# Kernel tuning notes

Measured on AMD Instinct MI355X. Metric: run time of the kernel, lower is better.

The kernel has to match this reference:

```python
import jax, jax.numpy as jnp
import numpy as np

D_MODEL = 768
D_STATE = 16
K_CONV = 4
BATCH = 2
SEQ = 2048


def setup_inputs() -> dict:
    key = jax.random.key(0)
    ks = jax.random.split(key, 16)
    dm, ds, K = D_MODEL, D_STATE, K_CONV
    s = 0.02
    inp = {
        "x": jax.random.normal(ks[0], (BATCH, SEQ, dm), dtype=jnp.float32),
        # linear weights stored (in, out); y = x @ W + b (equivalent to torch Linear)
        "Wi": jax.random.normal(ks[1], (dm, 2 * dm), dtype=jnp.float32) * s,
        "bi": jnp.zeros((2 * dm,), jnp.float32),
        "Wconv": jax.random.normal(ks[2], (dm, K), dtype=jnp.float32) * s,
        "bconv": jnp.zeros((dm,), jnp.float32),
        "Wdt": jax.random.normal(ks[3], (dm, dm), dtype=jnp.float32) * s,
        "bdt": jnp.zeros((dm,), jnp.float32),
        "WB": jax.random.normal(ks[4], (dm, dm * ds), dtype=jnp.float32) * s,
        "bB": jnp.zeros((dm * ds,), jnp.float32),
        "WC": jax.random.normal(ks[5], (dm, dm * ds), dtype=jnp.float32) * s,
        "bC": jnp.zeros((dm * ds,), jnp.float32),
        "A_log": jnp.zeros((dm, ds), jnp.float32),  # matches nn.Parameter(torch.zeros)
        "D": jnp.ones((dm,), jnp.float32),          # matches nn.Parameter(torch.ones)
        "Wo": jax.random.normal(ks[6], (dm, dm), dtype=jnp.float32) * s,
        "bo": jnp.zeros((dm,), jnp.float32),
    }
    return inp


def _forward(x, Wi, bi, Wconv, bconv, Wdt, bdt, WB, bB, WC, bC, A_log, D, Wo, bo):
    B, L, dm = x.shape
    ds = A_log.shape[1]
    K = Wconv.shape[1]

    uv = x @ Wi + bi                        # (B, L, 2*dm)
    u, v = uv[..., :dm], uv[..., dm:]

    # causal depthwise conv1d: torch pads K-1 both sides, keeps first L outputs
    u_pad = jnp.pad(u, ((0, 0), (K - 1, 0), (0, 0)))
    u_conv = bconv + sum(u_pad[:, k:k + L, :] * Wconv[:, k] for k in range(K))

    dt = jax.nn.softplus(u_conv @ Wdt + bdt)            # (B, L, dm)
    Bt = (u_conv @ WB + bB).reshape(B, L, dm, ds)       # (B, L, dm, ds)
    Ct = (u_conv @ WC + bC).reshape(B, L, dm, ds)
    A = -jnp.exp(A_log)                                  # (dm, ds)

    def step(s, inputs):
        dt_t, u_t, B_tt, C_tt = inputs                   # (B,dm), (B,dm), (B,dm,ds), (B,dm,ds)
        dt_e = dt_t[..., None]
        s = s * jnp.exp(dt_e * A) + dt_e * B_tt * u_t[..., None]
        y = jnp.sum(C_tt * s, axis=-1) + D * u_t         # (B, dm)
        return s, y

    s0 = jnp.zeros((B, dm, ds), x.dtype)
    xs = (dt.transpose(1, 0, 2), u_conv.transpose(1, 0, 2),
          Bt.transpose(1, 0, 2, 3), Ct.transpose(1, 0, 2, 3))
    _, ys = jax.lax.scan(step, s0, xs)                   # ys: (L, B, dm)
    y = ys.transpose(1, 0, 2)

    y = y * jax.nn.sigmoid(v)
    return y @ Wo + bo


def reference(x, Wi, bi, Wconv, bconv, Wdt, bdt, WB, bB, WC, bC, A_log, D, Wo, bo):
    return _forward(x, Wi, bi, Wconv, bconv, Wdt, bdt, WB, bB, WC, bC, A_log, D, Wo, bo)
```

## Files before the change

### kernel.cpp

```cpp
#include <hip/hip_runtime.h>

#define DM 768
#define DS 16
#define SEQ 2048
#define BATCH 2
#define MROWS (BATCH*SEQ)
#define N_UV (2*DM)
#define N_BC (DM*DS)
#define NGRP (BATCH*DM/4)
#define SUBMAX 64

typedef _Float16 half8 __attribute__((ext_vector_type(8)));
typedef float floatx4 __attribute__((ext_vector_type(4)));
typedef int i32x4 __attribute__((ext_vector_type(4)));
typedef unsigned short us8 __attribute__((ext_vector_type(8)));
typedef signed char c8 __attribute__((ext_vector_type(8)));

static __device__ __forceinline__ unsigned short f2h(float f) {
  _Float16 h = (_Float16)f;
  return __builtin_bit_cast(unsigned short, h);
}
static __device__ __forceinline__ float h2f(unsigned short u) {
  return (float)__builtin_bit_cast(_Float16, u);
}
static __device__ __forceinline__ float softplus_f(float x) {
  return (x > 20.f) ? x : log1pf(__expf(x));
}
static __device__ __forceinline__ void async_cp16(const void* g, void* l) {
  __builtin_amdgcn_global_load_lds(
      (const __attribute__((address_space(1))) void*)g,
      (__attribute__((address_space(3))) void*)l, 16, 0, 0);
}
static __device__ __forceinline__ float row_reduce16(float v) {
  int x;
  x = __builtin_amdgcn_update_dpp(0, __builtin_bit_cast(int, v), 0x128, 0xf, 0xf, true);
  v += __builtin_bit_cast(float, x);
  x = __builtin_amdgcn_update_dpp(0, __builtin_bit_cast(int, v), 0x124, 0xf, 0xf, true);
  v += __builtin_bit_cast(float, x);
  x = __builtin_amdgcn_update_dpp(0, __builtin_bit_cast(int, v), 0x122, 0xf, 0xf, true);
  v += __builtin_bit_cast(float, x);
  x = __builtin_amdgcn_update_dpp(0, __builtin_bit_cast(int, v), 0x121, 0xf, 0xf, true);
  v += __builtin_bit_cast(float, x);
  return v;
}

__global__ void convert_f2h(const float* __restrict__ in,
                            unsigned short* __restrict__ out, int n) {
  int i = (blockIdx.x * blockDim.x + threadIdx.x) * 4;
  if (i >= n) return;
  float4 f = *(const float4*)(in + i);
  ushort4 h;
  h.x = f2h(f.x); h.y = f2h(f.y); h.z = f2h(f.z); h.w = f2h(f.w);
  *(ushort4*)(out + i) = h;
}

__global__ void transpose_w5(const float* __restrict__ W0, const float* __restrict__ W1,
                             const float* __restrict__ W2, const float* __restrict__ W3,
                             const float* __restrict__ W4,
                             unsigned short* __restrict__ T0, unsigned short* __restrict__ T1,
                             unsigned short* __restrict__ T2, unsigned short* __restrict__ T3,
                             unsigned short* __restrict__ T4,
                             int N0, int N1, int N2, int N3, int N4) {
  const float* W; unsigned short* WT; int N;
  switch (blockIdx.z) {
    case 0: W = W0; WT = T0; N = N0; break;
    case 1: W = W1; WT = T1; N = N1; break;
    case 2: W = W2; WT = T2; N = N2; break;
    case 3: W = W3; WT = T3; N = N3; break;
    default: W = W4; WT = T4; N = N4; break;
  }
  int n0 = blockIdx.x * 32;
  if (n0 >= N) return;
  int k0 = blockIdx.y * 32;
  __shared__ float tile[32][33];
  int tx = threadIdx.x, ty = threadIdx.y;
#pragma unroll
  for (int i = 0; i < 32; i += 8)
    tile[ty + i][tx] = W[(size_t)(k0 + ty + i) * N + (n0 + tx)];
  __syncthreads();
  int kp = tx & 15, half = tx >> 4;
#pragma unroll
  for (int i = 0; i < 2; i++) {
    int nl = ty + half * 8 + i * 16;
    unsigned int pk = (unsigned int)f2h(tile[2 * kp][nl]) |
                      ((unsigned int)f2h(tile[2 * kp + 1][nl]) << 16);
    *(unsigned int*)&WT[(size_t)(n0 + nl) * DM + k0 + 2 * kp] = pk;
  }
}

__global__ __launch_bounds__(256)
void quant_rows(const unsigned short* __restrict__ in0,
                const unsigned short* __restrict__ in1,
                signed char* __restrict__ out0, signed char* __restrict__ out1,
                float* __restrict__ sc0, float* __restrict__ sc1, int R) {
  const unsigned short* in = blockIdx.y ? in1 : in0;
  signed char* out = blockIdx.y ? out1 : out0;
  float* scp = blockIdx.y ? sc1 : sc0;
  int row = blockIdx.x * 4 + (threadIdx.x >> 6);
  if (row >= R) return;
  int lane = threadIdx.x & 63;
  const us8* ch = (const us8*)(in + (size_t)row * DM);
  us8 a = ch[lane];
  us8 b = ch[64 + (lane & 31)];
  float fa[8], fb[8];
  float m = 0.f;
#pragma unroll
  for (int j = 0; j < 8; j++) { fa[j] = h2f(a[j]); m = fmaxf(m, fabsf(fa[j])); }
#pragma unroll
  for (int j = 0; j < 8; j++) fb[j] = h2f(b[j]);
  if (lane < 32) {
#pragma unroll
    for (int j = 0; j < 8; j++) m = fmaxf(m, fabsf(fb[j]));
  }
#pragma unroll
  for (int off = 32; off; off >>= 1) m = fmaxf(m, __shfl_xor(m, off));
  float inv = (m > 0.f) ? 127.f / m : 0.f;
  if (lane == 0) scp[row] = m * (1.f / 127.f);
  c8 qa, qb;
#pragma unroll
  for (int j = 0; j < 8; j++)
    qa[j] = (signed char)__float2int_rn(fminf(fmaxf(fa[j] * inv, -127.f), 127.f));
#pragma unroll
  for (int j = 0; j < 8; j++)
    qb[j] = (signed char)__float2int_rn(fminf(fmaxf(fb[j] * inv, -127.f), 127.f));
  c8* o = (c8*)(out + (size_t)row * DM);
  o[lane] = qa;
  if (lane < 32) o[64 + lane] = qb;
}

template<int ACT, int OUTH>
__global__ __launch_bounds__(256)
void gemm_f16(const unsigned short* __restrict__ A,
              const unsigned short* __restrict__ BT0,
              const unsigned short* __restrict__ BT1,
              const float* __restrict__ bias0,
              const float* __restrict__ bias1,
              void* __restrict__ Cout0,
              void* __restrict__ Cout1,
              int M, int N, int K, int TCa, int bstride, int row0) {
  const unsigned short* BT = blockIdx.z ? BT1 : BT0;
// ... 28 lines not shown
    async_cp16(Arow0 + k0, ldsA0);
    async_cp16(Arow1 + k0, ldsA1);
    async_cp16(Brow0 + k0, ldsB0);
    async_cp16(Brow1 + k0, ldsB1);
    __syncthreads();
    half8 af[4], bf[4];
#pragma unroll
    for (int i = 0; i < 4; i++) {
      af[i] = __builtin_bit_cast(half8, *(const uint4*)&As[(wm + i * 16 + l16) * 32 + pch]);
      bf[i] = __builtin_bit_cast(half8, *(const uint4*)&Bs[(wn + i * 16 + l16) * 32 + pch]);
    }
#pragma unroll
    for (int mi = 0; mi < 4; mi++)
#pragma unroll
      for (int ni = 0; ni < 4; ni++)
        acc[mi][ni] = __builtin_amdgcn_mfma_f32_16x16x32_f16(af[mi], bf[ni], acc[mi][ni], 0, 0, 0);
    __syncthreads();
  }

#pragma unroll
  for (int ni = 0; ni < 4; ni++) {
    int col = n0 + wn + ni * 16 + l16;
    float bv = bias[col];
#pragma unroll
    for (int mi = 0; mi < 4; mi++) {
#pragma unroll
      for (int r = 0; r < 4; r++) {
        int row = m0 + wm + mi * 16 + quad * 4 + r;
        float v = acc[mi][ni][r] + bv;
        if (ACT == 1) v = softplus_f(v);
        if (OUTH) ((unsigned short*)Cout)[(size_t)row * N + col] = f2h(v);
        else      ((float*)Cout)[(size_t)row * N + col] = v;
      }
    }
  }
}

__global__ __launch_bounds__(256)
void gemm_i8(const signed char* __restrict__ A,
             const signed char* __restrict__ BT0,
             const signed char* __restrict__ BT1,
             const float* __restrict__ bias0,
             const float* __restrict__ bias1,
             const float* __restrict__ sA,
             const float* __restrict__ sB0,
             const float* __restrict__ sB1,
             unsigned short* __restrict__ C0,
             unsigned short* __restrict__ C1,
             int M, int N, int K, int TCa, int bstride, int row0) {
  const signed char* BT = blockIdx.z ? BT1 : BT0;
  const float* bias = blockIdx.z ? bias1 : bias0;
  const float* sB = blockIdx.z ? sB1 : sB0;
  unsigned short* Cout = blockIdx.z ? C1 : C0;
  __shared__ __align__(16) signed char As[128 * 64];
  __shared__ __align__(16) signed char Bs[128 * 64];
  const int m0 = blockIdx.y * 128, n0 = blockIdx.x * 128;
  const int tid = threadIdx.x;
  const int lane = tid & 63, wave = tid >> 6;
  const int wm = (wave >> 1) * 64, wn = (wave & 1) * 64;
  const int l16 = lane & 15, quad = lane >> 4;
  const int sr = tid >> 2;
  const int sc = ((tid & 3) ^ ((tid >> 3) & 3)) * 16;
  const int pch = (quad ^ ((l16 >> 1) & 3)) * 16;

  i32x4 acc[4][4] = {};

  const int mA0 = m0 + sr, mA1 = m0 + sr + 64;
  const int gA0 = (mA0 / TCa) * bstride + row0 + (mA0 % TCa);
  const int gA1 = (mA1 / TCa) * bstride + row0 + (mA1 % TCa);
  const signed char* Arow0 = A + (size_t)gA0 * K + sc;
  const signed char* Arow1 = A + (size_t)gA1 * K + sc;
  const signed char* Brow0 = BT + (size_t)(n0 + sr) * K + sc;
  const signed char* Brow1 = BT + (size_t)(n0 + sr + 64) * K + sc;
  signed char* ldsA0 = As + (wave * 16) * 64;
  signed char* ldsA1 = As + (64 + wave * 16) * 64;
  signed char* ldsB0 = Bs + (wave * 16) * 64;
  signed char* ldsB1 = Bs + (64 + wave * 16) * 64;

  for (int k0 = 0; k0 < K; k0 += 64) {
    async_cp16(Arow0 + k0, ldsA0);
    async_cp16(Arow1 + k0, ldsA1);
    async_cp16(Brow0 + k0, ldsB0);
    async_cp16(Brow1 + k0, ldsB1);
    __syncthreads();
    i32x4 af[4], bf[4];
#pragma unroll
    for (int i = 0; i < 4; i++) {
      af[i] = *(const i32x4*)&As[(wm + i * 16 + l16) * 64 + pch];
      bf[i] = *(const i32x4*)&Bs[(wn + i * 16 + l16) * 64 + pch];
    }
#pragma unroll
    for (int mi = 0; mi < 4; mi++)
#pragma unroll
      for (int ni = 0; ni < 4; ni++)
        acc[mi][ni] = __builtin_amdgcn_mfma_i32_16x16x64_i8(af[mi], bf[ni], acc[mi][ni], 0, 0, 0);
    __syncthreads();
  }

  const int rowAbase = (m0 / TCa) * (bstride - TCa) + row0;
  float savs[4][4];
#pragma unroll
  for (int mi = 0; mi < 4; mi++)
#pragma unroll
    for (int r = 0; r < 4; r++)
      savs[mi][r] = sA[rowAbase + m0 + wm + mi * 16 + quad * 4 + r];

#pragma unroll
  for (int ni = 0; ni < 4; ni++) {
    int col = n0 + wn + ni * 16 + l16;
    float bv = bias[col];
    float sbv = sB[col];
#pragma unroll
    for (int mi = 0; mi < 4; mi++) {
#pragma unroll
      for (int r = 0; r < 4; r++) {
        int row = m0 + wm + mi * 16 + quad * 4 + r;
        float v = (float)acc[mi][ni][r] * (savs[mi][r] * sbv) + bv;
        Cout[(size_t)row * N + col] = f2h(v);
      }
    }
  }
}

__global__ void dwconv(const unsigned short* __restrict__ uv,
                       const float* __restrict__ Wconv,
                       const float* __restrict__ bconv,
                       unsigned short* __restrict__ uc) {
  int idx = blockIdx.x * 256 + threadIdx.x;
  int c = (idx % (DM / 2)) * 2;
  int row = idx / (DM / 2);
  int t = row & (SEQ - 1);
  float a0 = bconv[c], a1 = bconv[c + 1];
  const float* w0 = Wconv + c * 4;
  const float* w1 = Wconv + (c + 1) * 4;
#pragma unroll
  for (int k = 0; k < 4; k++) {
    int tt = t - 3 + k;
    if (tt >= 0) {
      ushort2 u2 = *(const ushort2*)&uv[(size_t)(row - 3 + k) * N_UV + c];
      a0 += h2f(u2.x) * w0[k];
      a1 += h2f(u2.y) * w1[k];
    }
  }
  ushort2 o; o.x = f2h(a0); o.y = f2h(a1);
  *(ushort2*)&uc[(size_t)row * DM + c] = o;
}

__global__ __launch_bounds__(64)
void scan_pass1(const unsigned short* __restrict__ dt,
                const unsigned short* __restrict__ uc,
                const unsigned short* __restrict__ Btc,
                const float* __restrict__ A_log,
                float* __restrict__ Ssub,
                float* __restrict__ Aexp,
                int ci, int TC, int SUBn) {
  const int TSUB = TC / SUBn;
  int wid = blockIdx.x, sub = blockIdx.y;
  int b = wid / (DM / 4);
  int c0 = (wid % (DM / 4)) * 4;
  int lane = threadIdx.x;
  int c = c0 + (lane >> 4);
  float Acj = -__expf(A_log[c0 * DS + lane]);
  int col = c0 * DS + lane;
  size_t gbase = (size_t)b * SEQ + (size_t)ci * TC + (size_t)sub * TSUB;
  size_t lbase = (size_t)b * TC + (size_t)sub * TSUB;

  float s = 0.f, dsum = 0.f;
  float n_dt[8], n_u[8], n_B[8];
#pragma unroll
  for (int i = 0; i < 8; i++) {
    n_dt[i] = h2f(dt[(gbase + i) * DM + c]);
    n_u[i]  = h2f(uc[(gbase + i) * DM + c]);
    n_B[i]  = h2f(Btc[(lbase + i) * N_BC + col]);
  }
  for (int t0 = 0; t0 < TSUB; t0 += 8) {
    float c_dt[8], c_u[8], c_B[8];
#pragma unroll
    for (int i = 0; i < 8; i++) { c_dt[i] = n_dt[i]; c_u[i] = n_u[i]; c_B[i] = n_B[i]; }
    if (t0 + 8 < TSUB) {
#pragma unroll
      for (int i = 0; i < 8; i++) {
        size_t gr = gbase + t0 + 8 + i, lr = lbase + t0 + 8 + i;
        n_dt[i] = h2f(dt[gr * DM + c]);
        n_u[i]  = h2f(uc[gr * DM + c]);
        n_B[i]  = h2f(Btc[lr * N_BC + col]);
      }
    }
#pragma unroll
    for (int i = 0; i < 8; i++) {
      float dtc = c_dt[i];
      dsum += dtc;
      float a = __expf(dtc * Acj);
      s = fmaf(s, a, dtc * c_B[i] * c_u[i]);
    }
  }
  int idx = (sub * BATCH + b) * N_BC + col;
  Ssub[idx] = s;
  Aexp[idx] = __expf(Acj * dsum);
}

template<int SUBN>
__global__ __launch_bounds__(64)
void scan_combine(const float* Ssub, const float* Aexp,
                  float* Sinit, float* s_state, int ci) {
  int wid = blockIdx.x;
  int b = wid / (DM / 4);
  int c0 = (wid % (DM / 4)) * 4;
  int col = c0 * DS + threadIdx.x;
  int sidx = b * N_BC + col;
  float sa[SUBN], ae[SUBN];
#pragma unroll
  for (int k = 0; k < SUBN; k++) {
    int idx = (k * BATCH + b) * N_BC + col;
    sa[k] = Ssub[idx];
    ae[k] = Aexp[idx];
  }
  float s = (ci == 0) ? 0.f : s_state[sidx];
#pragma unroll
  for (int k = 0; k < SUBN; k++) {
    int idx = (k * BATCH + b) * N_BC + col;
    Sinit[idx] = s;
    s = fmaf(s, ae[k], sa[k]);
  }
  s_state[sidx] = s;
}

__global__ __launch_bounds__(64)
void scan_pass2(const unsigned short* __restrict__ dt,
                const unsigned short* __restrict__ uc,
                const unsigned short* __restrict__ Btc,
                const unsigned short* __restrict__ Ctc,
                const unsigned short* __restrict__ uv,
                const float* __restrict__ A_log,
                const float* __restrict__ Dv,
                const float* __restrict__ Sinit,
                unsigned short* __restrict__ yg,
                int ci, int TC, int SUBn) {
  const int TSUB = TC / SUBn;
  int wid = blockIdx.x, sub = blockIdx.y;
  int b = wid / (DM / 4);
  int c0 = (wid % (DM / 4)) * 4;
  int lane = threadIdx.x;
  int j = lane & 15;
  int c = c0 + (lane >> 4);
  float Acj = -__expf(A_log[c0 * DS + lane]);
  float Dc = Dv[c];
  int col = c0 * DS + lane;
  float s = Sinit[(sub * BATCH + b) * N_BC + col];
  size_t gbase = (size_t)b * SEQ + (size_t)ci * TC + (size_t)sub * TSUB;
  size_t lbase = (size_t)b * TC + (size_t)sub * TSUB;

  float n_dt[8], n_u[8], n_B[8], n_C[8], n_v[8];
#pragma unroll
  for (int i = 0; i < 8; i++) {
    size_t gr = gbase + i, lr = lbase + i;
    n_dt[i] = h2f(dt[gr * DM + c]);
    n_u[i]  = h2f(uc[gr * DM + c]);
    n_B[i]  = h2f(Btc[lr * N_BC + col]);
    n_C[i]  = h2f(Ctc[lr * N_BC + col]);
    n_v[i]  = h2f(uv[gr * N_UV + DM + c]);
  }
  for (int t0 = 0; t0 < TSUB; t0 += 8) {
    float c_dt[8], c_u[8], c_B[8], c_C[8], c_v[8];
#pragma unroll
    for (int i = 0; i < 8; i++) {
      c_dt[i] = n_dt[i]; c_u[i] = n_u[i]; c_B[i] = n_B[i];
      c_C[i] = n_C[i]; c_v[i] = n_v[i];
    }
    if (t0 + 8 < TSUB) {
#pragma unroll
      for (int i = 0; i < 8; i++) {
        size_t gr = gbase + t0 + 8 + i, lr = lbase + t0 + 8 + i;
        n_dt[i] = h2f(dt[gr * DM + c]);
        n_u[i]  = h2f(uc[gr * DM + c]);
        n_B[i]  = h2f(Btc[lr * N_BC + col]);
        n_C[i]  = h2f(Ctc[lr * N_BC + col]);
        n_v[i]  = h2f(uv[gr * N_UV + DM + c]);
      }
    }
#pragma unroll
    for (int i = 0; i < 8; i++) {
      float dtc = c_dt[i];
      float a = __expf(dtc * Acj);
      s = fmaf(s, a, dtc * c_B[i] * c_u[i]);
      float yt = row_reduce16(c_C[i] * s);
      if (j == 0) {
        float y = yt + Dc * c_u[i];
        float g = 1.f / (1.f + __expf(-c_v[i]));
        yg[(gbase + t0 + i) * DM + c] = f2h(y * g);
      }
    }
  }
}

extern "C" void kernel_launch(void* const* d_in, const int* in_sizes, int n_in,
                              void* d_out, int out_size, void* d_ws, size_t ws_size,
                              hipStream_t stream) {
  const float* x     = (const float*)d_in[0];
  const float* Wi    = (const float*)d_in[1];
  const float* bi    = (const float*)d_in[2];
  const float* Wconv = (const float*)d_in[3];
  const float* bconv = (const float*)d_in[4];
  const float* Wdt   = (const float*)d_in[5];
  const float* bdt   = (const float*)d_in[6];
  const float* WB    = (const float*)d_in[7];
  const float* bB    = (const float*)d_in[8];
  const float* WC    = (const float*)d_in[9];
  const float* bC    = (const float*)d_in[10];
  const float* A_log = (const float*)d_in[11];
  const float* Dv    = (const float*)d_in[12];
  const float* Wo    = (const float*)d_in[13];
  const float* bo    = (const float*)d_in[14];
  float* out = (float*)d_out;
  (void)in_sizes; (void)n_in; (void)out_size;

  auto pad = [](size_t b) { return (b + 255) & ~(size_t)255; };

  const size_t sz_xb   = pad((size_t)MROWS * DM * 2);
  const size_t sz_WiT  = pad((size_t)N_UV * DM * 2);
  const size_t sz_WdtT = pad((size_t)DM * DM * 2);
  const size_t sz_WBT  = pad((size_t)N_BC * DM * 2);
  const size_t sz_WCT  = pad((size_t)N_BC * DM * 2);
  const size_t sz_WoT  = pad((size_t)DM * DM * 2);
  const size_t sz_uvb  = pad((size_t)MROWS * N_UV * 2);
  const size_t sz_ucb  = pad((size_t)MROWS * DM * 2);
  const size_t sz_dtb  = pad((size_t)MROWS * DM * 2);
  const size_t sz_st   = pad((size_t)BATCH * N_BC * 4);
  const size_t sz_sub  = pad((size_t)SUBMAX * BATCH * N_BC * 4);
  const size_t sz_uc8  = pad((size_t)MROWS * DM);
  const size_t sz_w8   = pad((size_t)N_BC * DM);
  const size_t sz_sA   = pad((size_t)MROWS * 4);
  const size_t sz_sB   = pad((size_t)N_BC * 4);
  const size_t fixed = sz_xb + sz_WiT + sz_WdtT + sz_WBT + sz_WCT + sz_WoT +
                       sz_uvb + sz_ucb + sz_dtb + sz_st + 2 * sz_sub +
                       sz_uc8 + 2 * sz_w8 + sz_sA + 2 * sz_sB;

  int NC = 16;
  for (int nc : {1, 2, 4, 8, 16}) {
    size_t need = fixed + 2 * pad((size_t)BATCH * (SEQ / nc) * N_BC * 2);
    if (need <= ws_size) { NC = nc; break; }
  }
  const int TC = SEQ / NC;
  const int MC = BATCH * TC;
  const int SUBn = (TC / 8 < SUBMAX) ? (TC / 8) : SUBMAX;

  char* ws = (char*)d_ws;
  size_t off = 0;
  auto alloc = [&](size_t bytes) { char* p = ws + off; off += bytes; return p; };
  unsigned short* xb   = (unsigned short*)alloc(sz_xb);
  unsigned short* WiT  = (unsigned short*)alloc(sz_WiT);
  unsigned short* WdtT = (unsigned short*)alloc(sz_WdtT);
  unsigned short* WBT  = (unsigned short*)alloc(sz_WBT);
  unsigned short* WCT  = (unsigned short*)alloc(sz_WCT);
  unsigned short* WoT  = (unsigned short*)alloc(sz_WoT);
  unsigned short* uvb  = (unsigned short*)alloc(sz_uvb);
  unsigned short* ucb  = (unsigned short*)alloc(sz_ucb);
  unsigned short* dtb  = (unsigned short*)alloc(sz_dtb);
  float*          sst  = (float*)alloc(sz_st);
  float*          Ssub = (float*)alloc(sz_sub);
  float*          Aexp = (float*)alloc(sz_sub);
  signed char*    uc8  = (signed char*)alloc(sz_uc8);
  signed char*    WBT8 = (signed char*)alloc(sz_w8);
  signed char*    WCT8 = (signed char*)alloc(sz_w8);
  float*          sAu  = (float*)alloc(sz_sA);
  float*          sB0  = (float*)alloc(sz_sB);
  float*          sB1  = (float*)alloc(sz_sB);
  unsigned short* Btc  = (unsigned short*)alloc(pad((size_t)MC * N_BC * 2));
  unsigned short* Ctc  = (unsigned short*)alloc(pad((size_t)MC * N_BC * 2));
  unsigned short* ygb  = xb;
  float*          Sini = Ssub;

  convert_f2h<<<dim3(MROWS * DM / 1024), dim3(256), 0, stream>>>(x, xb, MROWS * DM);
  transpose_w5<<<dim3(N_BC / 32, DM / 32, 5), dim3(32, 8), 0, stream>>>(
      Wi, Wdt, WB, WC, Wo, WiT, WdtT, WBT, WCT, WoT, N_UV, DM, N_BC, N_BC, DM);
  quant_rows<<<dim3(N_BC / 4, 2), 256, 0, stream>>>(WBT, WCT, WBT8, WCT8,
                                                    sB0, sB1, N_BC);

  gemm_f16<0, 1><<<dim3(N_UV / 128, MROWS / 128, 1), 256, 0, stream>>>(
      xb, WiT, WiT, bi, bi, uvb, uvb, MROWS, N_UV, DM, MROWS, 0, 0);
  dwconv<<<dim3(MROWS * DM / 512), 256, 0, stream>>>(uvb, Wconv, bconv, ucb);
  quant_rows<<<dim3(MROWS / 4, 1), 256, 0, stream>>>(ucb, ucb, uc8, uc8,
                                                     sAu, sAu, MROWS);
  gemm_f16<1, 1><<<dim3(DM / 128, MROWS / 128, 1), 256, 0, stream>>>(
      ucb, WdtT, WdtT, bdt, bdt, dtb, dtb, MROWS, DM, DM, MROWS, 0, 0);

  for (int ci = 0; ci < NC; ci++) {
    gemm_i8<<<dim3(N_BC / 128, MC / 128, 2), 256, 0, stream>>>(
        uc8, WBT8, WCT8, bB, bC, sAu, sB0, sB1, Btc, Ctc,
        MC, N_BC, DM, TC, SEQ, ci * TC);
    scan_pass1<<<dim3(NGRP, SUBn), 64, 0, stream>>>(dtb, ucb, Btc, A_log,
                                                    Ssub, Aexp, ci, TC, SUBn);
    switch (SUBn) {
      case 64: scan_combine<64><<<dim3(NGRP), 64, 0, stream>>>(Ssub, Aexp, Sini, sst, ci); break;
      case 32: scan_combine<32><<<dim3(NGRP), 64, 0, stream>>>(Ssub, Aexp, Sini, sst, ci); break;
      default: scan_combine<16><<<dim3(NGRP), 64, 0, stream>>>(Ssub, Aexp, Sini, sst, ci); break;
    }
    scan_pass2<<<dim3(NGRP, SUBn), 64, 0, stream>>>(dtb, ucb, Btc, Ctc, uvb,
                                                    A_log, Dv, Sini, ygb, ci, TC, SUBn);
  }

  gemm_f16<0, 0><<<dim3(DM / 128, MROWS / 128, 1), 256, 0, stream>>>(
      ygb, WoT, WoT, bo, bo, out, out, MROWS, DM, DM, MROWS, 0, 0);
}
```

Before: 553.6 us.

## Triple-buffer int8 GEMM LDS loads and vectorize transposed epilogue stores

```diff
diff --git a/kernel.cpp b/kernel.cpp
--- a/kernel.cpp
+++ b/kernel.cpp
@@ -15,6 +15,7 @@
 typedef int i32x4 __attribute__((ext_vector_type(4)));
 typedef unsigned short us8 __attribute__((ext_vector_type(8)));
 typedef signed char c8 __attribute__((ext_vector_type(8)));
+typedef __fp16 fp16x2 __attribute__((ext_vector_type(2)));
 
 static __device__ __forceinline__ unsigned short f2h(float f) {
   _Float16 h = (_Float16)f;
@@ -22,6 +23,10 @@
 }
 static __device__ __forceinline__ float h2f(unsigned short u) {
   return (float)__builtin_bit_cast(_Float16, u);
+}
+static __device__ __forceinline__ unsigned int pk2h(float a, float b) {
+  fp16x2 r = __builtin_amdgcn_cvt_pkrtz(a, b);
+  return __builtin_bit_cast(unsigned int, r);
 }
 static __device__ __forceinline__ float softplus_f(float x) {
   return (x > 20.f) ? x : log1pf(__expf(x));
@@ -220,8 +225,8 @@
   const float* bias = blockIdx.z ? bias1 : bias0;
   const float* sB = blockIdx.z ? sB1 : sB0;
   unsigned short* Cout = blockIdx.z ? C1 : C0;
-  __shared__ __align__(16) signed char As[128 * 64];
-  __shared__ __align__(16) signed char Bs[128 * 64];
+  __shared__ __align__(16) signed char As[3][128 * 64];
+  __shared__ __align__(16) signed char Bs[3][128 * 64];
   const int m0 = blockIdx.y * 128, n0 = blockIdx.x * 128;
   const int tid = threadIdx.x;
   const int lane = tid & 63, wave = tid >> 6;
@@ -240,52 +245,68 @@
   const signed char* Arow1 = A + (size_t)gA1 * K + sc;
   const signed char* Brow0 = BT + (size_t)(n0 + sr) * K + sc;
   const signed char* Brow1 = BT + (size_t)(n0 + sr + 64) * K + sc;
-  signed char* ldsA0 = As + (wave * 16) * 64;
-  signed char* ldsA1 = As + (64 + wave * 16) * 64;
-  signed char* ldsB0 = Bs + (wave * 16) * 64;
-  signed char* ldsB1 = Bs + (64 + wave * 16) * 64;
-
-  for (int k0 = 0; k0 < K; k0 += 64) {
-    async_cp16(Arow0 + k0, ldsA0);
-    async_cp16(Arow1 + k0, ldsA1);
-    async_cp16(Brow0 + k0, ldsB0);
-    async_cp16(Brow1 + k0, ldsB1);
-    __syncthreads();
+  const int woff = (wave * 16) * 64;
+
+  const int nt = K >> 6;
+  auto stage = [&](int t, int b) {
+    int k0 = t << 6;
+    async_cp16(Arow0 + k0, &As[b][woff]);
+    async_cp16(Arow1 + k0, &As[b][64 * 64 + woff]);
+    async_cp16(Brow0 + k0, &Bs[b][woff]);
+    async_cp16(Brow1 + k0, &Bs[b][64 * 64 + woff]);
+  };
+  stage(0, 0);
+  if (nt > 1) stage(1, 1);
+  int cur = 0;
+  for (int t = 0; t < nt; ++t) {
+    if (t + 2 < nt) {
+      int b2 = cur + 2; if (b2 >= 3) b2 -= 3;
+      stage(t + 2, b2);
+      asm volatile("s_waitcnt vmcnt(8)" ::: "memory");
+    } else if (t + 1 < nt) {
+      asm volatile("s_waitcnt vmcnt(4)" ::: "memory");
+    } else {
+      asm volatile("s_waitcnt vmcnt(0)" ::: "memory");
+    }
+    __builtin_amdgcn_s_barrier();
     i32x4 af[4], bf[4];
 #pragma unroll
     for (int i = 0; i < 4; i++) {
-      af[i] = *(const i32x4*)&As[(wm + i * 16 + l16) * 64 + pch];
-      bf[i] = *(const i32x4*)&Bs[(wn + i * 16 + l16) * 64 + pch];
-    }
+      af[i] = *(const i32x4*)&As[cur][(wm + i * 16 + l16) * 64 + pch];
+      bf[i] = *(const i32x4*)&Bs[cur][(wn + i * 16 + l16) * 64 + pch];
+    }
+    asm volatile("s_waitcnt lgkmcnt(0)" ::: "memory");
+    __builtin_amdgcn_s_barrier();
+    __builtin_amdgcn_s_setprio(1);
 #pragma unroll
     for (int mi = 0; mi < 4; mi++)
 #pragma unroll
       for (int ni = 0; ni < 4; ni++)
-        acc[mi][ni] = __builtin_amdgcn_mfma_i32_16x16x64_i8(af[mi], bf[ni], acc[mi][ni], 0, 0, 0);
-    __syncthreads();
+        acc[mi][ni] = __builtin_amdgcn_mfma_i32_16x16x64_i8(bf[ni], af[mi], acc[mi][ni], 0, 0, 0);
+    __builtin_amdgcn_s_setprio(0);
+    cur = (cur == 2) ? 0 : cur + 1;
   }
 
   const int rowAbase = (m0 / TCa) * (bstride - TCa) + row0;
-  float savs[4][4];
-#pragma unroll
-  for (int mi = 0; mi < 4; mi++)
-#pragma unroll
-    for (int r = 0; r < 4; r++)
-      savs[mi][r] = sA[rowAbase + m0 + wm + mi * 16 + quad * 4 + r];
-
-#pragma unroll
-  for (int ni = 0; ni < 4; ni++) {
-    int col = n0 + wn + ni * 16 + l16;
-    float bv = bias[col];
-    float sbv = sB[col];
-#pragma unroll
-    for (int mi = 0; mi < 4; mi++) {
-#pragma unroll
-      for (int r = 0; r < 4; r++) {
-        int row = m0 + wm + mi * 16 + quad * 4 + r;
-        float v = (float)acc[mi][ni][r] * (savs[mi][r] * sbv) + bv;
-        Cout[(size_t)row * N + col] = f2h(v);
-      }
+
+#pragma unroll
+  for (int mi = 0; mi < 4; mi++) {
+    int row = m0 + wm + mi * 16 + l16;
+    float sa = sA[rowAbase + row];
+    size_t outb = (size_t)row * N;
+#pragma unroll
+    for (int ni = 0; ni < 4; ni++) {
+      int nb = n0 + wn + ni * 16 + quad * 4;
+      float4 sb4 = *(const float4*)&sB[nb];
+      float4 bv4 = *(const float4*)&bias[nb];
+      float v0 = (float)acc[mi][ni][0] * (sa * sb4.x) + bv4.x;
+      float v1 = (float)acc[mi][ni][1] * (sa * sb4.y) + bv4.y;
+      float v2 = (float)acc[mi][ni][2] * (sa * sb4.z) + bv4.z;
+      float v3 = (float)acc[mi][ni][3] * (sa * sb4.w) + bv4.w;
+      uint2 pk;
+      pk.x = pk2h(v0, v1);
+      pk.y = pk2h(v2, v3);
+      *(uint2*)&Cout[outb + nb] = pk;
     }
   }
 }
```

After: 584.9 us. +5.7%, slower.

## Transpose scan activations to channel-major and vectorize int8 GEMM epilogue stores

Applied to the files above, without the earlier changes.

```diff
diff --git a/kernel.cpp b/kernel.cpp
--- a/kernel.cpp
+++ b/kernel.cpp
@@ -15,6 +15,7 @@
 typedef int i32x4 __attribute__((ext_vector_type(4)));
 typedef unsigned short us8 __attribute__((ext_vector_type(8)));
 typedef signed char c8 __attribute__((ext_vector_type(8)));
+typedef __fp16 fp16x2 __attribute__((ext_vector_type(2)));
 
 static __device__ __forceinline__ unsigned short f2h(float f) {
   _Float16 h = (_Float16)f;
@@ -22,6 +23,10 @@
 }
 static __device__ __forceinline__ float h2f(unsigned short u) {
   return (float)__builtin_bit_cast(_Float16, u);
+}
+static __device__ __forceinline__ unsigned int pk2h(float a, float b) {
+  fp16x2 r = __builtin_amdgcn_cvt_pkrtz(a, b);
+  return __builtin_bit_cast(unsigned int, r);
 }
 static __device__ __forceinline__ float softplus_f(float x) {
   return (x > 20.f) ? x : log1pf(__expf(x));
@@ -86,6 +91,30 @@
                       ((unsigned int)f2h(tile[2 * kp + 1][nl]) << 16);
     *(unsigned int*)&WT[(size_t)(n0 + nl) * DM + k0 + 2 * kp] = pk;
   }
+}
+
+__global__ void transpose_act3(const unsigned short* __restrict__ dt,
+                               const unsigned short* __restrict__ uc,
+                               const unsigned short* __restrict__ uv,
+                               unsigned short* __restrict__ dtT,
+                               unsigned short* __restrict__ ucT,
+                               unsigned short* __restrict__ vT) {
+  const unsigned short* src; unsigned short* dst; int ld, coff;
+  switch (blockIdx.z) {
+    case 0:  src = dt; dst = dtT; ld = DM;   coff = 0;  break;
+    case 1:  src = uc; dst = ucT; ld = DM;   coff = 0;  break;
+    default: src = uv; dst = vT;  ld = N_UV; coff = DM; break;
+  }
+  __shared__ unsigned short tile[32][33];
+  int r0 = blockIdx.x * 32, c0 = blockIdx.y * 32;
+  int tx = threadIdx.x, ty = threadIdx.y;
+#pragma unroll
+  for (int i = 0; i < 32; i += 8)
+    tile[ty + i][tx] = src[(size_t)(r0 + ty + i) * ld + coff + c0 + tx];
+  __syncthreads();
+#pragma unroll
+  for (int i = 0; i < 32; i += 8)
+    dst[(size_t)(c0 + ty + i) * MROWS + r0 + tx] = tile[tx][ty + i];
 }
 
 __global__ __launch_bounds__(256)
@@ -261,31 +290,30 @@
     for (int mi = 0; mi < 4; mi++)
 #pragma unroll
       for (int ni = 0; ni < 4; ni++)
-        acc[mi][ni] = __builtin_amdgcn_mfma_i32_16x16x64_i8(af[mi], bf[ni], acc[mi][ni], 0, 0, 0);
+        acc[mi][ni] = __builtin_amdgcn_mfma_i32_16x16x64_i8(bf[ni], af[mi], acc[mi][ni], 0, 0, 0);
     __syncthreads();
   }
 
   const int rowAbase = (m0 / TCa) * (bstride - TCa) + row0;
-  float savs[4][4];
-#pragma unroll
-  for (int mi = 0; mi < 4; mi++)
-#pragma unroll
-    for (int r = 0; r < 4; r++)
-      savs[mi][r] = sA[rowAbase + m0 + wm + mi * 16 + quad * 4 + r];
-
-#pragma unroll
-  for (int ni = 0; ni < 4; ni++) {
-    int col = n0 + wn + ni * 16 + l16;
-    float bv = bias[col];
-    float sbv = sB[col];
-#pragma unroll
-    for (int mi = 0; mi < 4; mi++) {
-#pragma unroll
-      for (int r = 0; r < 4; r++) {
-        int row = m0 + wm + mi * 16 + quad * 4 + r;
-        float v = (float)acc[mi][ni][r] * (savs[mi][r] * sbv) + bv;
-        Cout[(size_t)row * N + col] = f2h(v);
-      }
+
+#pragma unroll
+  for (int mi = 0; mi < 4; mi++) {
+    int row = m0 + wm + mi * 16 + l16;
+    float sa = sA[rowAbase + row];
+    size_t outb = (size_t)row * N;
+#pragma unroll
+    for (int ni = 0; ni < 4; ni++) {
+      int nb = n0 + wn + ni * 16 + quad * 4;
+      float4 sb4 = *(const float4*)&sB[nb];
+      float4 bv4 = *(const float4*)&bias[nb];
+      float v0 = (float)acc[mi][ni][0] * (sa * sb4.x) + bv4.x;
+      float v1 = (float)acc[mi][ni][1] * (sa * sb4.y) + bv4.y;
+      float v2 = (float)acc[mi][ni][2] * (sa * sb4.z) + bv4.z;
+      float v3 = (float)acc[mi][ni][3] * (sa * sb4.w) + bv4.w;
+      uint2 pk;
+      pk.x = pk2h(v0, v1);
+      pk.y = pk2h(v2, v3);
+      *(uint2*)&Cout[outb + nb] = pk;
     }
   }
 }
@@ -314,52 +342,53 @@
   *(ushort2*)&uc[(size_t)row * DM + c] = o;
 }
 
-__global__ __launch_bounds__(64)
-void scan_pass1(const unsigned short* __restrict__ dt,
-                const unsigned short* __restrict__ uc,
+__global__ __launch_bounds__(256)
+void scan_pass1(const unsigned short* __restrict__ dtT,
+                const unsigned short* __restrict__ ucT,
                 const unsigned short* __restrict__ Btc,
                 const float* __restrict__ A_log,
                 float* __restrict__ Ssub,
                 float* __restrict__ Aexp,
                 int ci, int TC, int SUBn) {
   const int TSUB = TC / SUBn;
-  int wid = blockIdx.x, sub = blockIdx.y;
+  int wid = blockIdx.x * 4 + (threadIdx.x >> 6);
+  int sub = blockIdx.y;
   int b = wid / (DM / 4);
   int c0 = (wid % (DM / 4)) * 4;
-  int lane = threadIdx.x;
+  int lane = threadIdx.x & 63;
   int c = c0 + (lane >> 4);
   float Acj = -__expf(A_log[c0 * DS + lane]);
   int col = c0 * DS + lane;
-  size_t gbase = (size_t)b * SEQ + (size_t)ci * TC + (size_t)sub * TSUB;
+  size_t tbase = (size_t)b * SEQ + (size_t)ci * TC + (size_t)sub * TSUB;
   size_t lbase = (size_t)b * TC + (size_t)sub * TSUB;
+  const unsigned short* dtp = dtT + (size_t)c * MROWS + tbase;
+  const unsigned short* ucp = ucT + (size_t)c * MROWS + tbase;
 
   float s = 0.f, dsum = 0.f;
-  float n_dt[8], n_u[8], n_B[8];
-#pragma unroll
-  for (int i = 0; i < 8; i++) {
-    n_dt[i] = h2f(dt[(gbase + i) * DM + c]);
-    n_u[i]  = h2f(uc[(gbase + i) * DM + c]);
-    n_B[i]  = h2f(Btc[(lbase + i) * N_BC + col]);
-  }
+  us8 ndt = *(const us8*)dtp;
+  us8 nuc = *(const us8*)ucp;
+  float n_B[8];
+#pragma unroll
+  for (int i = 0; i < 8; i++)
+    n_B[i] = h2f(Btc[(lbase + i) * N_BC + col]);
   for (int t0 = 0; t0 < TSUB; t0 += 8) {
-    float c_dt[8], c_u[8], c_B[8];
-#pragma unroll
-    for (int i = 0; i < 8; i++) { c_dt[i] = n_dt[i]; c_u[i] = n_u[i]; c_B[i] = n_B[i]; }
+    us8 cdt = ndt, cuc = nuc;
+    float c_B[8];
+#pragma unroll
+    for (int i = 0; i < 8; i++) c_B[i] = n_B[i];
     if (t0 + 8 < TSUB) {
-#pragma unroll
-      for (int i = 0; i < 8; i++) {
-        size_t gr = gbase + t0 + 8 + i, lr = lbase + t0 + 8 + i;
-        n_dt[i] = h2f(dt[gr * DM + c]);
-        n_u[i]  = h2f(uc[gr * DM + c]);
-        n_B[i]  = h2f(Btc[lr * N_BC + col]);
-      }
+      ndt = *(const us8*)&dtp[t0 + 8];
+      nuc = *(const us8*)&ucp[t0 + 8];
+#pragma unroll
+      for (int i = 0; i < 8; i++)
+        n_B[i] = h2f(Btc[(lbase + t0 + 8 + i) * N_BC + col]);
     }
 #pragma unroll
     for (int i = 0; i < 8; i++) {
-      float dtc = c_dt[i];
+      float dtc = h2f(cdt[i]);
       dsum += dtc;
       float a = __expf(dtc * Acj);
-      s = fmaf(s, a, dtc * c_B[i] * c_u[i]);
+      s = fmaf(s, a, dtc * c_B[i] * h2f(cuc[i]));
     }
   }
   int idx = (sub * BATCH + b) * N_BC + col;
@@ -368,13 +397,14 @@
 }
 
 template<int SUBN>
-__global__ __launch_bounds__(64)
+__global__ __launch_bounds__(256)
 void scan_combine(const float* Ssub, const float* Aexp,
                   float* Sinit, float* s_state, int ci) {
-  int wid = blockIdx.x;
+  int wid = blockIdx.x * 4 + (threadIdx.x >> 6);
+  int lane = threadIdx.x & 63;
   int b = wid / (DM / 4);
   int c0 = (wid % (DM / 4)) * 4;
-  int col = c0 * DS + threadIdx.x;
+  int col = c0 * DS + lane;
   int sidx = b * N_BC + col;
   float sa[SUBN], ae[SUBN];
 #pragma unroll
@@ -393,69 +423,72 @@
   s_state[sidx] = s;
 }
 
-__global__ __launch_bounds__(64)
-void scan_pass2(const unsigned short* __restrict__ dt,
-                const unsigned short* __restrict__ uc,
+__global__ __launch_bounds__(256)
+void scan_pass2(const unsigned short* __restrict__ dtT,
+                const unsigned short* __restrict__ ucT,
                 const unsigned short* __restrict__ Btc,
                 const unsigned short* __restrict__ Ctc,
-                const unsigned short* __restrict__ uv,
+                const unsigned short* __restrict__ vT,
                 const float* __restrict__ A_log,
                 const float* __restrict__ Dv,
                 const float* __restrict__ Sinit,
                 unsigned short* __restrict__ yg,
                 int ci, int TC, int SUBn) {
   const int TSUB = TC / SUBn;
-  int wid = blockIdx.x, sub = blockIdx.y;
+  int wid = blockIdx.x * 4 + (threadIdx.x >> 6);
+  int sub = blockIdx.y;
   int b = wid / (DM / 4);
   int c0 = (wid % (DM / 4)) * 4;
-  int lane = threadIdx.x;
+  int lane = threadIdx.x & 63;
   int j = lane & 15;
   int c = c0 + (lane >> 4);
   float Acj = -__expf(A_log[c0 * DS + lane]);
   float Dc = Dv[c];
   int col = c0 * DS + lane;
   float s = Sinit[(sub * BATCH + b) * N_BC + col];
-  size_t gbase = (size_t)b * SEQ + (size_t)ci * TC + (size_t)sub * TSUB;
+  size_t tbase = (size_t)b * SEQ + (size_t)ci * TC + (size_t)sub * TSUB;
   size_t lbase = (size_t)b * TC + (size_t)sub * TSUB;
-
-  float n_dt[8], n_u[8], n_B[8], n_C[8], n_v[8];
+  const unsigned short* dtp = dtT + (size_t)c * MROWS + tbase;
+  const unsigned short* ucp = ucT + (size_t)c * MROWS + tbase;
+  const unsigned short* vp  = vT  + (size_t)c * MROWS + tbase;
+
+  us8 ndt = *(const us8*)dtp;
+  us8 nuc = *(const us8*)ucp;
+  us8 nv  = *(const us8*)vp;
+  float n_B[8], n_C[8];
 #pragma unroll
   for (int i = 0; i < 8; i++) {
-    size_t gr = gbase + i, lr = lbase + i;
-    n_dt[i] = h2f(dt[gr * DM + c]);
-    n_u[i]  = h2f(uc[gr * DM + c]);
-    n_B[i]  = h2f(Btc[lr * N_BC + col]);
-    n_C[i]  = h2f(Ctc[lr * N_BC + col]);
-    n_v[i]  = h2f(uv[gr * N_UV + DM + c]);
+    size_t lr = lbase + i;
+    n_B[i] = h2f(Btc[lr * N_BC + col]);
+    n_C[i] = h2f(Ctc[lr * N_BC + col]);
   }
   for (int t0 = 0; t0 < TSUB; t0 += 8) {
-    float c_dt[8], c_u[8], c_B[8], c_C[8], c_v[8];
+    us8 cdt = ndt, cuc = nuc, cv = nv;
+    float c_B[8], c_C[8];
+#pragma unroll
+    for (int i = 0; i < 8; i++) { c_B[i] = n_B[i]; c_C[i] = n_C[i]; }
+    if (t0 + 8 < TSUB) {
+      ndt = *(const us8*)&dtp[t0 + 8];
+      nuc = *(const us8*)&ucp[t0 + 8];
+      nv  = *(const us8*)&vp[t0 + 8];
+#pragma unroll
+      for (int i = 0; i < 8; i++) {
+        size_t lr = lbase + t0 + 8 + i;
+        n_B[i] = h2f(Btc[lr * N_BC + col]);
+        n_C[i] = h2f(Ctc[lr * N_BC + col]);
+      }
+    }
 #pragma unroll
     for (int i = 0; i < 8; i++) {
-      c_dt[i] = n_dt[i]; c_u[i] = n_u[i]; c_B[i] = n_B[i];
-      c_C[i] = n_C[i]; c_v[i] = n_v[i];
-    }
-    if (t0 + 8 < TSUB) {
-#pragma unroll
-      for (int i = 0; i < 8; i++) {
-        size_t gr = gbase + t0 + 8 + i, lr = lbase + t0 + 8 + i;
-        n_dt[i] = h2f(dt[gr * DM + c]);
-        n_u[i]  = h2f(uc[gr * DM + c]);
-        n_B[i]  = h2f(Btc[lr * N_BC + col]);
-        n_C[i]  = h2f(Ctc[lr * N_BC + col]);
-        n_v[i]  = h2f(uv[gr * N_UV + DM + c]);
-      }
-    }
-#pragma unroll
-    for (int i = 0; i < 8; i++) {
-      float dtc = c_dt[i];
+      float dtc = h2f(cdt[i]);
+      float uci = h2f(cuc[i]);
       float a = __expf(dtc * Acj);
-      s = fmaf(s, a, dtc * c_B[i] * c_u[i]);
+      s = fmaf(s, a, dtc * c_B[i] * uci);
       float yt = row_reduce16(c_C[i] * s);
       if (j == 0) {
-        float y = yt + Dc * c_u[i];
-        float g = 1.f / (1.f + __expf(-c_v[i]));
-        yg[(gbase + t0 + i) * DM + c] = f2h(y * g);
+        float y = yt + Dc * uci;
+        float g = 1.f / (1.f + __expf(-h2f(cv[i])));
+        yg[(tbase + t0 + i) * DM + c] = f2h(y * g);
       }
     }
   }
@@ -493,6 +526,7 @@
   const size_t sz_uvb  = pad((size_t)MROWS * N_UV * 2);
   const size_t sz_ucb  = pad((size_t)MROWS * DM * 2);
   const size_t sz_dtb  = pad((size_t)MROWS * DM * 2);
+  const size_t sz_actT = pad((size_t)DM * MROWS * 2);
   const size_t sz_st   = pad((size_t)BATCH * N_BC * 4);
   const size_t sz_sub  = pad((size_t)SUBMAX * BATCH * N_BC * 4);
   const size_t sz_uc8  = pad((size_t)MROWS * DM);
@@ -500,8 +534,8 @@
   const size_t sz_sA   = pad((size_t)MROWS * 4);
   const size_t sz_sB   = pad((size_t)N_BC * 4);
   const size_t fixed = sz_xb + sz_WiT + sz_WdtT + sz_WBT + sz_WCT + sz_WoT +
-                       sz_uvb + sz_ucb + sz_dtb + sz_st + 2 * sz_sub +
-                       sz_uc8 + 2 * sz_w8 + sz_sA + 2 * sz_sB;
+                       sz_uvb + sz_ucb + sz_dtb + 3 * sz_actT + sz_st +
+                       2 * sz_sub + sz_uc8 + 2 * sz_w8 + sz_sA + 2 * sz_sB;
 
   int NC = 16;
   for (int nc : {1, 2, 4, 8, 16}) {
@@ -524,6 +558,9 @@
   unsigned short* uvb  = (unsigned short*)alloc(sz_uvb);
   unsigned short* ucb  = (unsigned short*)alloc(sz_ucb);
   unsigned short* dtb  = (unsigned short*)alloc(sz_dtb);
+  unsigned short* dtT  = (unsigned short*)alloc(sz_actT);
+  unsigned short* ucT  = (unsigned short*)alloc(sz_actT);
+  unsigned short* vT   = (unsigned short*)alloc(sz_actT);
   float*          sst  = (float*)alloc(sz_st);
   float*          Ssub = (float*)alloc(sz_sub);
   float*          Aexp = (float*)alloc(sz_sub);
@@ -551,20 +588,22 @@
                                                      sAu, sAu, MROWS);
   gemm_f16<1, 1><<<dim3(DM / 128, MROWS / 128, 1), 256, 0, stream>>>(
       ucb, WdtT, WdtT, bdt, bdt, dtb, dtb, MROWS, DM, DM, MROWS, 0, 0);
+  transpose_act3<<<dim3(MROWS / 32, DM / 32, 3), dim3(32, 8), 0, stream>>>(
+      dtb, ucb, uvb, dtT, ucT, vT);
 
   for (int ci = 0; ci < NC; ci++) {
     gemm_i8<<<dim3(N_BC / 128, MC / 128, 2), 256, 0, stream>>>(
         uc8, WBT8, WCT8, bB, bC, sAu, sB0, sB1, Btc, Ctc,
         MC, N_BC, DM, TC, SEQ, ci * TC);
-    scan_pass1<<<dim3(NGRP, SUBn), 64, 0, stream>>>(dtb, ucb, Btc, A_log,
-                                                    Ssub, Aexp, ci, TC, SUBn);
+    scan_pass1<<<dim3(NGRP / 4, SUBn), 256, 0, stream>>>(dtT, ucT, Btc, A_log,
+                                                         Ssub, Aexp, ci, TC, SUBn);
     switch (SUBn) {
-      case 64: scan_combine<64><<<dim3(NGRP), 64, 0, stream>>>(Ssub, Aexp, Sini, sst, ci); break;
-      case 32: scan_combine<32><<<dim3(NGRP), 64, 0, stream>>>(Ssub, Aexp, Sini, sst, ci); break;
-      default: scan_combine<16><<<dim3(NGRP), 64, 0, stream>>>(Ssub, Aexp, Sini, sst, ci); break;
-    }
-    scan_pass2<<<dim3(NGRP, SUBn), 64, 0, stream>>>(dtb, ucb, Btc, Ctc, uvb,
-                                                    A_log, Dv, Sini, ygb, ci, TC, SUBn);
+      case 64: scan_combine<64><<<dim3(NGRP / 4), 256, 0, stream>>>(Ssub, Aexp, Sini, sst, ci); break;
+      case 32: scan_combine<32><<<dim3(NGRP / 4), 256, 0, stream>>>(Ssub, Aexp, Sini, sst, ci); break;
+      default: scan_combine<16><<<dim3(NGRP / 4), 256, 0, stream>>>(Ssub, Aexp, Sini, sst, ci); break;
+    }
+    scan_pass2<<<dim3(NGRP / 4, SUBn), 256, 0, stream>>>(dtT, ucT, Btc, Ctc, vT,
+                                                         A_log, Dv, Sini, ygb, ci, TC, SUBn);
   }
 
   gemm_f16<0, 0><<<dim3(DM / 128, MROWS / 128, 1), 256, 0, stream>>>(
```

After: 590.5 us. +6.7%, slower.

## Replace chunked three-pass scan with single sequential scan over transposed activations

Applied to the files above, without the earlier changes.

```diff
diff --git a/kernel.cpp b/kernel.cpp
--- a/kernel.cpp
+++ b/kernel.cpp
@@ -8,7 +8,6 @@
 #define N_UV (2*DM)
 #define N_BC (DM*DS)
 #define NGRP (BATCH*DM/4)
-#define SUBMAX 64
 
 typedef _Float16 half8 __attribute__((ext_vector_type(8)));
 typedef float floatx4 __attribute__((ext_vector_type(4)));
@@ -86,6 +85,30 @@
                       ((unsigned int)f2h(tile[2 * kp + 1][nl]) << 16);
     *(unsigned int*)&WT[(size_t)(n0 + nl) * DM + k0 + 2 * kp] = pk;
   }
+}
+
+__global__ void transpose_act3(const unsigned short* __restrict__ dt,
+                               const unsigned short* __restrict__ uc,
+                               const unsigned short* __restrict__ uv,
+                               unsigned short* __restrict__ dtT,
+                               unsigned short* __restrict__ ucT,
+                               unsigned short* __restrict__ vT) {
+  const unsigned short* src; unsigned short* dst; int ld, coff;
+  switch (blockIdx.z) {
+    case 0:  src = dt; dst = dtT; ld = DM;   coff = 0;  break;
+    case 1:  src = uc; dst = ucT; ld = DM;   coff = 0;  break;
+    default: src = uv; dst = vT;  ld = N_UV; coff = DM; break;
+  }
+  __shared__ unsigned short tile[32][33];
+  int r0 = blockIdx.x * 32, c0 = blockIdx.y * 32;
+  int tx = threadIdx.x, ty = threadIdx.y;
+#pragma unroll
+  for (int i = 0; i < 32; i += 8)
+    tile[ty + i][tx] = src[(size_t)(r0 + ty + i) * ld + coff + c0 + tx];
+  __syncthreads();
+#pragma unroll
+  for (int i = 0; i < 32; i += 8)
+    dst[(size_t)(c0 + ty + i) * MROWS + r0 + tx] = tile[tx][ty + i];
 }
 
 __global__ __launch_bounds__(256)
@@ -315,97 +338,17 @@
 }
 
 __global__ __launch_bounds__(64)
-void scan_pass1(const unsigned short* __restrict__ dt,
-                const unsigned short* __restrict__ uc,
-                const unsigned short* __restrict__ Btc,
-                const float* __restrict__ A_log,
-                float* __restrict__ Ssub,
-                float* __restrict__ Aexp,
-                int ci, int TC, int SUBn) {
-  const int TSUB = TC / SUBn;
-  int wid = blockIdx.x, sub = blockIdx.y;
-  int b = wid / (DM / 4);
-  int c0 = (wid % (DM / 4)) * 4;
-  int lane = threadIdx.x;
-  int c = c0 + (lane >> 4);
-  float Acj = -__expf(A_log[c0 * DS + lane]);
-  int col = c0 * DS + lane;
-  size_t gbase = (size_t)b * SEQ + (size_t)ci * TC + (size_t)sub * TSUB;
-  size_t lbase = (size_t)b * TC + (size_t)sub * TSUB;
-
-  float s = 0.f, dsum = 0.f;
-  float n_dt[8], n_u[8], n_B[8];
-#pragma unroll
-  for (int i = 0; i < 8; i++) {
-    n_dt[i] = h2f(dt[(gbase + i) * DM + c]);
-    n_u[i]  = h2f(uc[(gbase + i) * DM + c]);
-    n_B[i]  = h2f(Btc[(lbase + i) * N_BC + col]);
-  }
-  for (int t0 = 0; t0 < TSUB; t0 += 8) {
-    float c_dt[8], c_u[8], c_B[8];
-#pragma unroll
-    for (int i = 0; i < 8; i++) { c_dt[i] = n_dt[i]; c_u[i] = n_u[i]; c_B[i] = n_B[i]; }
-    if (t0 + 8 < TSUB) {
-#pragma unroll
-      for (int i = 0; i < 8; i++) {
-        size_t gr = gbase + t0 + 8 + i, lr = lbase + t0 + 8 + i;
-        n_dt[i] = h2f(dt[gr * DM + c]);
-        n_u[i]  = h2f(uc[gr * DM + c]);
-        n_B[i]  = h2f(Btc[lr * N_BC + col]);
-      }
-    }
-#pragma unroll
-    for (int i = 0; i < 8; i++) {
-      float dtc = c_dt[i];
-      dsum += dtc;
-      float a = __expf(dtc * Acj);
-      s = fmaf(s, a, dtc * c_B[i] * c_u[i]);
-    }
-  }
-  int idx = (sub * BATCH + b) * N_BC + col;
-  Ssub[idx] = s;
-  Aexp[idx] = __expf(Acj * dsum);
-}
-
-template<int SUBN>
-__global__ __launch_bounds__(64)
-void scan_combine(const float* Ssub, const float* Aexp,
-                  float* Sinit, float* s_state, int ci) {
+void scan_full(const unsigned short* __restrict__ dtT,
+               const unsigned short* __restrict__ ucT,
+               const unsigned short* __restrict__ vT,
+               const unsigned short* __restrict__ Btc,
+               const unsigned short* __restrict__ Ctc,
+               const float* __restrict__ A_log,
+               const float* __restrict__ Dv,
+               float* __restrict__ s_state,
+               unsigned short* __restrict__ yg,
+               int ci, int TC) {
   int wid = blockIdx.x;
-  int b = wid / (DM / 4);
-  int c0 = (wid % (DM / 4)) * 4;
-  int col = c0 * DS + threadIdx.x;
-  int sidx = b * N_BC + col;
-  float sa[SUBN], ae[SUBN];
-#pragma unroll
-  for (int k = 0; k < SUBN; k++) {
-    int idx = (k * BATCH + b) * N_BC + col;
-    sa[k] = Ssub[idx];
-    ae[k] = Aexp[idx];
-  }
-  float s = (ci == 0) ? 0.f : s_state[sidx];
-#pragma unroll
-  for (int k = 0; k < SUBN; k++) {
-    int idx = (k * BATCH + b) * N_BC + col;
-    Sinit[idx] = s;
-    s = fmaf(s, ae[k], sa[k]);
-  }
-  s_state[sidx] = s;
-}
-
-__global__ __launch_bounds__(64)
-void scan_pass2(const unsigned short* __restrict__ dt,
-                const unsigned short* __restrict__ uc,
-                const unsigned short* __restrict__ Btc,
-                const unsigned short* __restrict__ Ctc,
-                const unsigned short* __restrict__ uv,
-                const float* __restrict__ A_log,
-                const float* __restrict__ Dv,
-                const float* __restrict__ Sinit,
-                unsigned short* __restrict__ yg,
-                int ci, int TC, int SUBn) {
-  const int TSUB = TC / SUBn;
-  int wid = blockIdx.x, sub = blockIdx.y;
   int b = wid / (DM / 4);
   int c0 = (wid % (DM / 4)) * 4;
   int lane = threadIdx.x;
@@ -414,51 +357,57 @@
   float Acj = -__expf(A_log[c0 * DS + lane]);
   float Dc = Dv[c];
   int col = c0 * DS + lane;
-  float s = Sinit[(sub * BATCH + b) * N_BC + col];
-  size_t gbase = (size_t)b * SEQ + (size_t)ci * TC + (size_t)sub * TSUB;
-  size_t lbase = (size_t)b * TC + (size_t)sub * TSUB;
-
-  float n_dt[8], n_u[8], n_B[8], n_C[8], n_v[8];
-#pragma unroll
-  for (int i = 0; i < 8; i++) {
-    size_t gr = gbase + i, lr = lbase + i;
-    n_dt[i] = h2f(dt[gr * DM + c]);
-    n_u[i]  = h2f(uc[gr * DM + c]);
-    n_B[i]  = h2f(Btc[lr * N_BC + col]);
-    n_C[i]  = h2f(Ctc[lr * N_BC + col]);
-    n_v[i]  = h2f(uv[gr * N_UV + DM + c]);
-  }
-  for (int t0 = 0; t0 < TSUB; t0 += 8) {
-    float c_dt[8], c_u[8], c_B[8], c_C[8], c_v[8];
-#pragma unroll
-    for (int i = 0; i < 8; i++) {
-      c_dt[i] = n_dt[i]; c_u[i] = n_u[i]; c_B[i] = n_B[i];
-      c_C[i] = n_C[i]; c_v[i] = n_v[i];
-    }
-    if (t0 + 8 < TSUB) {
-#pragma unroll
-      for (int i = 0; i < 8; i++) {
-        size_t gr = gbase + t0 + 8 + i, lr = lbase + t0 + 8 + i;
-        n_dt[i] = h2f(dt[gr * DM + c]);
-        n_u[i]  = h2f(uc[gr * DM + c]);
-        n_B[i]  = h2f(Btc[lr * N_BC + col]);
-        n_C[i]  = h2f(Ctc[lr * N_BC + col]);
-        n_v[i]  = h2f(uv[gr * N_UV + DM + c]);
+  int sidx = b * N_BC + col;
+  float s = (ci == 0) ? 0.f : s_state[sidx];
+  size_t tbase = (size_t)b * SEQ + (size_t)ci * TC;
+  size_t lbase = (size_t)b * TC;
+  const unsigned short* dtp = dtT + (size_t)c * MROWS + tbase;
+  const unsigned short* ucp = ucT + (size_t)c * MROWS + tbase;
+  const unsigned short* vp  = vT  + (size_t)c * MROWS + tbase;
+
+  us8 adt[2], auc[2], avv[2];  float aB[16], aC[16];
+  us8 bdt[2], buc[2], bvv[2];  float bB[16], bC[16];
+
+  auto loadblk = [&](us8* d8, us8* u8, us8* v8, float* Bf, float* Cf, int t_) {
+    d8[0] = *(const us8*)&dtp[t_];
+    d8[1] = *(const us8*)&dtp[t_ + 8];
+    u8[0] = *(const us8*)&ucp[t_];
+    u8[1] = *(const us8*)&ucp[t_ + 8];
+    v8[0] = *(const us8*)&vp[t_];
+    v8[1] = *(const us8*)&vp[t_ + 8];
+#pragma unroll
+    for (int i = 0; i < 16; i++) {
+      size_t lr = lbase + t_ + i;
+      Bf[i] = h2f(Btc[lr * N_BC + col]);
+      Cf[i] = h2f(Ctc[lr * N_BC + col]);
+    }
+  };
+  auto compblk = [&](const us8* d8, const us8* u8, const us8* v8,
+                     const float* Bf, const float* Cf, int t_) {
+#pragma unroll
+    for (int i = 0; i < 16; i++) {
+      float dtc = h2f(d8[i >> 3][i & 7]);
+      float uci = h2f(u8[i >> 3][i & 7]);
+      float a = __expf(dtc * Acj);
+      s = fmaf(s, a, dtc * Bf[i] * uci);
+      float yt = row_reduce16(Cf[i] * s);
+      if (j == 0) {
+        float y = yt + Dc * uci;
+        float g = 1.f / (1.f + __expf(-h2f(v8[i >> 3][i & 7])));
+        yg[(tbase + t_ + i) * DM + c] = f2h(y * g);
       }
     }
-#pragma unroll
-    for (int i = 0; i < 8; i++) {
-      float dtc = c_dt[i];
-      float a = __expf(dtc * Acj);
-      s = fmaf(s, a, dtc * c_B[i] * c_u[i]);
-      float yt = row_reduce16(c_C[i] * s);
-      if (j == 0) {
-        float y = yt + Dc * c_u[i];
-        float g = 1.f / (1.f + __expf(-c_v[i]));
-        yg[(gbase + t0 + i) * DM + c] = f2h(y * g);
-      }
-    }
-  }
+  };
+
+  loadblk(adt, auc, avv, aB, aC, 0);
+  for (int t0 = 0; t0 < TC; t0 += 32) {
+    loadblk(bdt, buc, bvv, bB, bC, t0 + 16);
+    compblk(adt, auc, avv, aB, aC, t0);
+    if (t0 + 32 < TC)
+      loadblk(adt, auc, avv, aB, aC, t0 + 32);
+    compblk(bdt, buc, bvv, bB, bC, t0 + 16);
+  }
+  s_state[sidx] = s;
 }
 
 extern "C" void kernel_launch(void* const* d_in, const int* in_sizes, int n_in,
@@ -493,14 +442,14 @@
   const size_t sz_uvb  = pad((size_t)MROWS * N_UV * 2);
   const size_t sz_ucb  = pad((size_t)MROWS * DM * 2);
   const size_t sz_dtb  = pad((size_t)MROWS * DM * 2);
+  const size_t sz_actT = pad((size_t)DM * MROWS * 2);
   const size_t sz_st   = pad((size_t)BATCH * N_BC * 4);
-  const size_t sz_sub  = pad((size_t)SUBMAX * BATCH * N_BC * 4);
   const size_t sz_uc8  = pad((size_t)MROWS * DM);
   const size_t sz_w8   = pad((size_t)N_BC * DM);
   const size_t sz_sA   = pad((size_t)MROWS * 4);
   const size_t sz_sB   = pad((size_t)N_BC * 4);
   const size_t fixed = sz_xb + sz_WiT + sz_WdtT + sz_WBT + sz_WCT + sz_WoT +
-                       sz_uvb + sz_ucb + sz_dtb + sz_st + 2 * sz_sub +
+                       sz_uvb + sz_ucb + sz_dtb + 3 * sz_actT + sz_st +
                        sz_uc8 + 2 * sz_w8 + sz_sA + 2 * sz_sB;
 
   int NC = 16;
@@ -510,7 +459,6 @@
   }
   const int TC = SEQ / NC;
   const int MC = BATCH * TC;
-  const int SUBn = (TC / 8 < SUBMAX) ? (TC / 8) : SUBMAX;
 
   char* ws = (char*)d_ws;
   size_t off = 0;
@@ -524,9 +472,10 @@
   unsigned short* uvb  = (unsigned short*)alloc(sz_uvb);
   unsigned short* ucb  = (unsigned short*)alloc(sz_ucb);
   unsigned short* dtb  = (unsigned short*)alloc(sz_dtb);
+  unsigned short* dtT  = (unsigned short*)alloc(sz_actT);
+  unsigned short* ucT  = (unsigned short*)alloc(sz_actT);
+  unsigned short* vT   = (unsigned short*)alloc(sz_actT);
   float*          sst  = (float*)alloc(sz_st);
-  float*          Ssub = (float*)alloc(sz_sub);
-  float*          Aexp = (float*)alloc(sz_sub);
   signed char*    uc8  = (signed char*)alloc(sz_uc8);
   signed char*    WBT8 = (signed char*)alloc(sz_w8);
   signed char*    WCT8 = (signed char*)alloc(sz_w8);
@@ -536,7 +485,6 @@
   unsigned short* Btc  = (unsigned short*)alloc(pad((size_t)MC * N_BC * 2));
   unsigned short* Ctc  = (unsigned short*)alloc(pad((size_t)MC * N_BC * 2));
   unsigned short* ygb  = xb;
-  float*          Sini = Ssub;
 
   convert_f2h<<<dim3(MROWS * DM / 1024), dim3(256), 0, stream>>>(x, xb, MROWS * DM);
   transpose_w5<<<dim3(N_BC / 32, DM / 32, 5), dim3(32, 8), 0, stream>>>(
@@ -551,20 +499,15 @@
                                                      sAu, sAu, MROWS);
   gemm_f16<1, 1><<<dim3(DM / 128, MROWS / 128, 1), 256, 0, stream>>>(
       ucb, WdtT, WdtT, bdt, bdt, dtb, dtb, MROWS, DM, DM, MROWS, 0, 0);
+  transpose_act3<<<dim3(MROWS / 32, DM / 32, 3), dim3(32, 8), 0, stream>>>(
+      dtb, ucb, uvb, dtT, ucT, vT);
 
   for (int ci = 0; ci < NC; ci++) {
     gemm_i8<<<dim3(N_BC / 128, MC / 128, 2), 256, 0, stream>>>(
         uc8, WBT8, WCT8, bB, bC, sAu, sB0, sB1, Btc, Ctc,
         MC, N_BC, DM, TC, SEQ, ci * TC);
-    scan_pass1<<<dim3(NGRP, SUBn), 64, 0, stream>>>(dtb, ucb, Btc, A_log,
-                                                    Ssub, Aexp, ci, TC, SUBn);
-    switch (SUBn) {
-      case 64: scan_combine<64><<<dim3(NGRP), 64, 0, stream>>>(Ssub, Aexp, Sini, sst, ci); break;
-      case 32: scan_combine<32><<<dim3(NGRP), 64, 0, stream>>>(Ssub, Aexp, Sini, sst, ci); break;
-      default: scan_combine<16><<<dim3(NGRP), 64, 0, stream>>>(Ssub, Aexp, Sini, sst, ci); break;
-    }
-    scan_pass2<<<dim3(NGRP, SUBn), 64, 0, stream>>>(dtb, ucb, Btc, Ctc, uvb,
-                                                    A_log, Dv, Sini, ygb, ci, TC, SUBn);
+    scan_full<<<dim3(NGRP), 64, 0, stream>>>(dtT, ucT, vT, Btc, Ctc,
+                                             A_log, Dv, sst, ygb, ci, TC);
   }
 
   gemm_f16<0, 0><<<dim3(DM / 128, MROWS / 128, 1), 256, 0, stream>>>(
```

Measured after the change: 1.142 ms. 2.06x slower.
